# Performance work log

Hardware: AMD Instinct MI355X
Metric: run time of the kernel (lower is better)

## Reference

```python
import jax, jax.numpy as jnp
import numpy as np

B, C, D, H, W = 2, 512, 32, 32, 32
L, CTX = 256, 768
NH, HD, G = 8, 64, 8
EPS = 1e-5


def group_norm(x, w, b):
    Bb, Cc, Dd, Hh, Ww = x.shape
    xg = x.reshape(Bb, G, Cc // G, Dd, Hh, Ww)
    mu = xg.mean(axis=(2, 3, 4, 5), keepdims=True)
    var = xg.var(axis=(2, 3, 4, 5), keepdims=True)
    xn = ((xg - mu) * jax.lax.rsqrt(var + EPS)).reshape(Bb, Cc, Dd, Hh, Ww)
    return xn * w[None, :, None, None, None] + b[None, :, None, None, None]


def layer_norm(x, w, b):
    mu = x.mean(axis=-1, keepdims=True)
    var = x.var(axis=-1, keepdims=True)
    return (x - mu) * jax.lax.rsqrt(var + EPS) * w + b


def setup_inputs() -> dict:
    key = jax.random.key(0)
    ks = jax.random.split(key, 8)
    s = 0.02  # weight init scale
    return {
        "x": jax.random.normal(ks[0], (B, C, D, H, W), jnp.float32),
        "context": jax.random.normal(ks[1], (B, L, CTX), jnp.float32),
        "gn_w": jnp.ones((C,), jnp.float32),
        "gn_b": jnp.zeros((C,), jnp.float32),
        "ln_w": jnp.ones((CTX,), jnp.float32),
        "ln_b": jnp.zeros((CTX,), jnp.float32),
        "q_w": jax.random.normal(ks[2], (C, C), jnp.float32) * s,
        "q_b": jnp.zeros((C,), jnp.float32),
        "k_w": jax.random.normal(ks[3], (C, CTX), jnp.float32) * s,
        "k_b": jnp.zeros((C,), jnp.float32),
        "v_w": jax.random.normal(ks[4], (C, CTX), jnp.float32) * s,
        "v_b": jnp.zeros((C,), jnp.float32),
        "proj_w": jax.random.normal(ks[5], (C, C), jnp.float32) * s,
        "proj_b": jnp.zeros((C,), jnp.float32),
    }


def reference(x, context, gn_w, gn_b, ln_w, ln_b, q_w, q_b, k_w, k_b, v_w, v_b, proj_w, proj_b):
    Bb, Cc, Dd, Hh, Ww = x.shape
    S = Dd * Hh * Ww
    h = group_norm(x, gn_w, gn_b)
    ctx = layer_norm(context, ln_w, ln_b)
    # 1x1 Conv3d == per-voxel linear over channels
    q = jnp.einsum('oc,bcdhw->bodhw', q_w, h) + q_b[None, :, None, None, None]
    q = q.reshape(Bb, NH, HD, S)                                        # (b,h,e,s)
    k = (ctx @ k_w.T + k_b).reshape(Bb, L, NH, HD).transpose(0, 2, 1, 3)  # (b,h,l,e)
    v = (ctx @ v_w.T + v_b).reshape(Bb, L, NH, HD).transpose(0, 2, 1, 3)  # (b,h,l,e)
    scale = HD ** -0.5
    attn = jnp.einsum('bhes,bhle->bhsl', q, k) * scale                  # (b,h,S,L)
    attn = jax.nn.softmax(attn, axis=-1)
    out = jnp.einsum('bhsl,bhle->bhes', attn, v).reshape(Bb, Cc, Dd, Hh, Ww)
    out = jnp.einsum('oc,bcdhw->bodhw', proj_w, out) + proj_b[None, :, None, None, None]
    return out + x
```

## Files before the change

kernel.cpp:

```cpp
#include <hip/hip_runtime.h>

typedef unsigned short u16;
typedef unsigned int u32;
typedef __attribute__((ext_vector_type(4))) float f32x4;
typedef __attribute__((ext_vector_type(8))) short bf16x8;
typedef __attribute__((ext_vector_type(8))) u16 u16x8;
typedef __attribute__((ext_vector_type(4))) u16 u16x4;
typedef __attribute__((ext_vector_type(4))) u32 u32x4;

#define DEVI __device__ __forceinline__

constexpr int C_ = 512, S_ = 32768, L_ = 256, CTX_ = 768;

DEVI u16 f2b(float f) {
    union { float f; unsigned u; } x; x.f = f;
    unsigned r = x.u + 0x7fffu + ((x.u >> 16) & 1u);
    return (u16)(r >> 16);
}

DEVI f32x4 mfma16(bf16x8 a, bf16x8 b, f32x4 c) {
    return __builtin_amdgcn_mfma_f32_16x16x32_bf16(a, b, c, 0, 0, 0);
}

DEVI void gload16(const void* g, void* l) {
    __builtin_amdgcn_global_load_lds(
        (const __attribute__((address_space(1))) void*)g,
        (__attribute__((address_space(3))) void*)l, 16, 0, 0);
}

DEVI u32 cvtpk(float lo, float hi) {
    u32 d;
    asm("v_cvt_pk_bf16_f32 %0, %1, %2" : "=v"(d) : "v"(lo), "v"(hi));
    return d;
}
DEVI void pl32(u32& a, u32& b) {
    asm volatile("v_permlane32_swap_b32 %0, %1" : "+v"(a), "+v"(b));
}
DEVI void pl16(u32& a, u32& b) {
    asm volatile("v_permlane16_swap_b32 %0, %1" : "+v"(a), "+v"(b));
}

__global__ __launch_bounds__(256) void cvt_w(
    const float* __restrict__ a0, const float* __restrict__ a1,
    const float* __restrict__ a2, const float* __restrict__ a3,
    u16* __restrict__ o0, u16* __restrict__ o1,
    u16* __restrict__ o2, u16* __restrict__ o3)
{
    int which = blockIdx.y;
    const float* src = which == 0 ? a0 : which == 1 ? a1 : which == 2 ? a2 : a3;
    u16* dst = which == 0 ? o0 : which == 1 ? o1 : which == 2 ? o2 : o3;
    int n4 = (which == 1 || which == 2) ? (512 * 768 / 4) : (512 * 512 / 4);
    int i = blockIdx.x * 256 + threadIdx.x;
    if (i < n4) {
        float4 v = ((const float4*)src)[i];
        u16x4 o; o[0] = f2b(v.x); o[1] = f2b(v.y); o[2] = f2b(v.z); o[3] = f2b(v.w);
        ((u16x4*)dst)[i] = o;
    }
}

__global__ __launch_bounds__(256) void gn_partial(const float* __restrict__ x,
                                                  float* __restrict__ part)
{
    const int bg = blockIdx.y, blk = blockIdx.x, tid = threadIdx.x;
    const float* base = x + (size_t)bg * 64 * S_ + (size_t)blk * 1024 + tid * 4;
    float s1 = 0.f, s2 = 0.f;
    for (int c = 0; c < 64; ++c) {
        float4 v = *(const float4*)(base + (size_t)c * S_);
        s1 += v.x + v.y + v.z + v.w;
        s2 += v.x * v.x + v.y * v.y + v.z * v.z + v.w * v.w;
    }
    for (int m = 1; m < 64; m <<= 1) { s1 += __shfl_xor(s1, m); s2 += __shfl_xor(s2, m); }
    __shared__ float a1[4], a2[4];
    int w = tid >> 6, lane = tid & 63;
    if (lane == 0) { a1[w] = s1; a2[w] = s2; }
    __syncthreads();
    if (tid == 0) {
        part[(bg * 32 + blk) * 2 + 0] = a1[0] + a1[1] + a1[2] + a1[3];
        part[(bg * 32 + blk) * 2 + 1] = a2[0] + a2[1] + a2[2] + a2[3];
    }
}

__global__ __launch_bounds__(64) void gn_final(const float* __restrict__ part,
                                               float* __restrict__ stats)
{
    int bg = blockIdx.x, tid = threadIdx.x;
    float s1 = tid < 32 ? part[(bg * 32 + tid) * 2] : 0.f;
    float s2 = tid < 32 ? part[(bg * 32 + tid) * 2 + 1] : 0.f;
    for (int m = 1; m < 32; m <<= 1) { s1 += __shfl_xor(s1, m); s2 += __shfl_xor(s2, m); }
    if (tid == 0) {
        const float invN = 1.0f / (64.0f * (float)S_);
        float mu = s1 * invN, var = s2 * invN - mu * mu;
        stats[bg * 2] = mu;
        stats[bg * 2 + 1] = rsqrtf(var + 1e-5f);
    }
}

__global__ __launch_bounds__(256) void gn_coef(
    const float* __restrict__ stats, const float* __restrict__ gw,
    const float* __restrict__ gb, float* __restrict__ ca, float* __restrict__ cb)
{
    int i = blockIdx.x * 256 + threadIdx.x;
    int z = i >> 9, c = i & 511;
    int bg = z * 8 + (c >> 6);
    float mu = stats[bg * 2], rs = stats[bg * 2 + 1];
    float a = rs * gw[c];
    ca[i] = a;
    cb[i] = gb[c] - mu * a;
}

__global__ __launch_bounds__(256) void ln_ctx(
    const float* __restrict__ ctx, const float* __restrict__ lw,
    const float* __restrict__ lb, u16* __restrict__ cn)
{
    const int row = blockIdx.x, tid = threadIdx.x;
    const float* p = ctx + (size_t)row * CTX_;
    float v0 = p[tid], v1 = p[tid + 256], v2 = p[tid + 512];
    float s1 = v0 + v1 + v2, s2 = v0 * v0 + v1 * v1 + v2 * v2;
    for (int m = 1; m < 64; m <<= 1) { s1 += __shfl_xor(s1, m); s2 += __shfl_xor(s2, m); }
    __shared__ float a1[4], a2[4];
    int w = tid >> 6, lane = tid & 63;
    if (lane == 0) { a1[w] = s1; a2[w] = s2; }
    __syncthreads();
    s1 = a1[0] + a1[1] + a1[2] + a1[3];
    s2 = a2[0] + a2[1] + a2[2] + a2[3];
    const float invN = 1.0f / 768.0f;
    float mu = s1 * invN, rstd = rsqrtf(s2 * invN - mu * mu + 1e-5f);
    u16* o = cn + (size_t)row * CTX_;
    o[tid]       = f2b((v0 - mu) * rstd * lw[tid]       + lb[tid]);
    o[tid + 256] = f2b((v1 - mu) * rstd * lw[tid + 256] + lb[tid + 256]);
    o[tid + 512] = f2b((v2 - mu) * rstd * lw[tid + 512] + lb[tid + 512]);
}

template <int MODE, bool SWAP>
__global__ __launch_bounds__(256, 4) void gemm_nt(
    const u16* __restrict__ A, const u16* __restrict__ Bp,
    const float* __restrict__ bias, void* __restrict__ outp,
    const float* __restrict__ resid, int K, int ldo,
    size_t aStride, size_t bStride, size_t oStride, float scale,
    const u16* __restrict__ Bp2, const float* __restrict__ bias2,
    void* __restrict__ outp2)
{
    __shared__ __align__(16) u16 lA[2][4096];
    __shared__ __align__(16) u16 lB[2][4096];
    const int tid = threadIdx.x;
    const int w = tid >> 6, lane = tid & 63;
    const int g = lane >> 4, r = lane & 15;

    const int nx = gridDim.x, nxy = nx * gridDim.y;
    const int raw = blockIdx.x + nx * blockIdx.y;
    const int tile = (raw & 7) * (nxy >> 3) + (raw >> 3);
    const int bx = tile % nx, by = tile / nx;
    const int m0 = (SWAP ? by : bx) * 128, n0 = (SWAP ? bx : by) * 128;
    const int z = blockIdx.z;
    A += (size_t)z * aStride;
    const u16* Bsel = Bp;
    if constexpr (MODE == 3) { if (z) Bsel = Bp2; }
    Bsel += (size_t)z * bStride;

    const int l8 = lane & 7, lh = lane >> 3;
    const int u_ = l8 ^ lh;
    const int mro = (lh << 1) + (u_ >> 2);
    const int kco = (u_ & 3) * 8;
    const int wr = w >> 1, wc = w & 1;
    const int nt = K >> 5;

    f32x4 acc[4][4];
#pragma unroll
    for (int m = 0; m < 4; ++m)
#pragma unroll
        for (int n = 0; n < 4; ++n) acc[m][n] = f32x4{0.f, 0.f, 0.f, 0.f};

#define STAGE_B(t, bi_) {                                                      \
    size_t ko_ = (size_t)((t) * 32 + kco);                                     \
    _Pragma("unroll")                                                          \
    for (int j = 0; j < 2; ++j) {                                              \
        int grow_ = w * 32 + j * 16 + mro;                                     \
        gload16(Bsel + (size_t)(n0 + grow_) * K + ko_,                         \
                &lB[bi_][(w * 16 + j * 8) << 6]);                              \
    } }

#define STAGE_A(t, bi_) {                                                      \
    size_t ko_ = (size_t)((t) * 32 + kco);                                     \
    _Pragma("unroll")                                                          \
    for (int j = 0; j < 2; ++j) {                                              \
        int grow_ = w * 32 + j * 16 + mro;                                     \
        gload16(A + (size_t)(m0 + grow_) * K + ko_,                            \
                &lA[bi_][(w * 16 + j * 8) << 6]);                              \
    } }

    const float* xA = nullptr;
    const float* cAp = nullptr;
    const float* cBp = nullptr;
    int cp2 = 0, sb = 0, zc = 0;
    f32x4 a00{}, a01{}, a10{}, a11{};
    float2 ka{}, kb{};
    if constexpr (MODE == 4) {
        xA = resid + (size_t)z * ((size_t)C_ * S_);
        cAp = bias2;
        cBp = (const float*)outp2;
        cp2 = (tid >> 4) * 2;
        sb = (tid & 15) * 8;
        zc = z * 512;
    }

#define LOAD_A4(t) {                                                           \
    int c0n_ = (t) * 32 + cp2;                                                 \
    const float* r0_ = xA + (size_t)c0n_ * S_ + m0 + sb;                       \
    a00 = *(const f32x4*)r0_;  a01 = *(const f32x4*)(r0_ + 4);                 \
    a10 = *(const f32x4*)(r0_ + S_); a11 = *(const f32x4*)(r0_ + S_ + 4);      \
    ka = *(const float2*)&cAp[zc + c0n_];                                      \
    kb = *(const float2*)&cBp[zc + c0n_]; }

#define WRITE_A4(bi_) {                                                        \
    _Pragma("unroll")                                                          \
    for (int j = 0; j < 8; ++j) {                                              \
        float v0_ = ((j < 4) ? a00[j] : a01[j - 4]) * ka.x + kb.x;             \
        float v1_ = ((j < 4) ? a10[j] : a11[j - 4]) * ka.y + kb.y;             \
        int mm_ = sb + j;                                                      \
        int idx_ = ((mm_ >> 1) << 6)                                           \
            + (((((mm_ & 1) << 2) + (cp2 >> 3)) ^ ((mm_ >> 1) & 7)) << 3)      \
            + (cp2 & 7);                                                       \
        *(u32*)&lA[bi_][idx_] = cvtpk(v0_, v1_);                               \
    } }

    if constexpr (MODE == 4) {
        STAGE_B(0, 0);
        LOAD_A4(0);
        WRITE_A4(0);
    } else {
        STAGE_A(0, 0);
        STAGE_B(0, 0);
    }
    __syncthreads();

    for (int t = 0; t < nt; ++t) {
        const int cur = t & 1;
        if (t + 1 < nt) {
            STAGE_B(t + 1, cur ^ 1);
            if constexpr (MODE == 4) { LOAD_A4(t + 1); }
            else                     { STAGE_A(t + 1, cur ^ 1); }
        }
        bf16x8 af[4], bf_[4];
#pragma unroll
        for (int m = 0; m < 4; ++m) {
            int row = wr * 32 + m * 8 + (r >> 1);
            int slot = (((r & 1) << 2) + g) ^ ((r >> 1) & 7);
            af[m] = *(const bf16x8*)&lA[cur][(row << 6) + (slot << 3)];
        }
#pragma unroll
        for (int n = 0; n < 4; ++n) {
            int row = wc * 32 + n * 8 + (r >> 1);
            int slot = (((r & 1) << 2) + g) ^ ((r >> 1) & 7);
            bf_[n] = *(const bf16x8*)&lB[cur][(row << 6) + (slot << 3)];
        }
#pragma unroll
        for (int m = 0; m < 4; ++m)
#pragma unroll
            for (int n = 0; n < 4; ++n)
                acc[m][n] = mfma16(bf_[n], af[m], acc[m][n]);
        if constexpr (MODE == 4) { if (t + 1 < nt) WRITE_A4(cur ^ 1); }
        __syncthreads();
    }
#undef STAGE_A
#undef STAGE_B
#undef LOAD_A4
#undef WRITE_A4

    if constexpr (MODE == 0 || MODE == 4) {
        u16* ob = (u16*)outp + (size_t)z * oStride;
#pragma unroll
        for (int m = 0; m < 4; ++m) {
            int gm = m0 + wr * 64 + m * 16 + r;
#pragma unroll
            for (int n = 0; n < 4; ++n) {
                int gn0 = n0 + wc * 64 + n * 16 + g * 4;
                float4 bn = *(const float4*)&bias[gn0];
                u32 w0 = cvtpk(acc[m][n][0] * scale + bn.x * scale,
                               acc[m][n][1] * scale + bn.y * scale);
                u32 w1 = cvtpk(acc[m][n][2] * scale + bn.z * scale,
                               acc[m][n][3] * scale + bn.w * scale);
                *(uint2*)&ob[(size_t)gm * ldo + gn0] = make_uint2(w0, w1);
            }
        }
    } else if constexpr (MODE == 2) {
        float* of = (float*)outp + (size_t)z * oStride;
        const float* rs = resid + (size_t)z * oStride;
#pragma unroll
        for (int m = 0; m < 4; ++m) {
            int gm = m0 + wr * 64 + m * 16 + r;
            float bm = bias[gm];
#pragma unroll
            for (int n = 0; n < 4; ++n) {
                int gn0 = n0 + wc * 64 + n * 16 + g * 4;
                size_t idx = (size_t)gm * ldo + gn0;
                float4 rv = *(const float4*)&rs[idx];
                float4 o4;
                o4.x = acc[m][n][0] + bm + rv.x;
                o4.y = acc[m][n][1] + bm + rv.y;
                o4.z = acc[m][n][2] + bm + rv.z;
                o4.w = acc[m][n][3] + bm + rv.w;
                *(float4*)&of[idx] = o4;
            }
        }
    } else if constexpr (MODE == 3) {
        if (z == 0) {
            u16* ob = (u16*)outp;
#pragma unroll
            for (int m = 0; m < 4; ++m) {
                int gm = m0 + wr * 64 + m * 16 + r;
#pragma unroll
                for (int n = 0; n < 4; ++n) {
                    int gn0 = n0 + wc * 64 + n * 16 + g * 4;
                    float4 bn = *(const float4*)&bias[gn0];
                    u32 w0 = cvtpk(acc[m][n][0] + bn.x, acc[m][n][1] + bn.y);
                    u32 w1 = cvtpk(acc[m][n][2] + bn.z, acc[m][n][3] + bn.w);
                    *(uint2*)&ob[(size_t)gm * ldo + gn0] = make_uint2(w0, w1);
                }
            }
        } else {
            u16* ob = (u16*)outp2;
#pragma unroll
            for (int m = 0; m < 4; ++m) {
                int gm = m0 + wr * 64 + m * 16 + r;
                int bb = gm >> 8, l = gm & 255;
#pragma unroll
                for (int n = 0; n < 4; ++n) {
                    int gn0 = n0 + wc * 64 + n * 16 + g * 4;
#pragma unroll
                    for (int i = 0; i < 4; ++i)
                        ob[((size_t)(bb * 512 + gn0 + i)) * 256 + l] =
                            f2b(acc[m][n][i] + bias2[gn0 + i]);
                }
            }
        }
    }
}

__global__ __launch_bounds__(256, 2) void attn_kernel(
    const u16* __restrict__ q, const u16* __restrict__ kk,
    const u16* __restrict__ vv, u16* __restrict__ ao)
{
    __shared__ __align__(16) u16 sm[32768];
    const int tid = threadIdx.x;
    const int w = tid >> 6, lane = tid & 63;
    const int g = lane >> 4, r = lane & 15;
    const int bh = blockIdx.y, b = bh >> 3, h = bh & 7;
    const int s0 = blockIdx.x * 128;

    {
        const u16* kbase = kk + ((size_t)b * L_) * C_ + h * 64;
#pragma unroll
        for (int j = 0; j < 8; ++j) {
            int idx = j * 256 + tid;
            int l = idx >> 3, ch = idx & 7;
            u16x8 val = *(const u16x8*)(kbase + (size_t)l * C_ + ch * 8);
            *(u16x8*)&sm[l * 64 + ((ch ^ (l & 7)) << 3)] = val;
        }
        const u16* vbase = vv + ((size_t)bh * 64) * 256;
#pragma unroll
        for (int j = 0; j < 8; ++j) {
            int idx = j * 256 + tid;
            int e = idx >> 5, ch = idx & 31;
            u16x8 val = *(const u16x8*)(vbase + (size_t)e * 256 + ch * 8);
            *(u16x8*)&sm[16384 + e * 256 + ((ch ^ (e & 7)) << 3)] = val;
        }
    }

    const int sw = s0 + w * 32;
    bf16x8 qf[2][2];
#pragma unroll
    for (int m = 0; m < 2; ++m)
#pragma unroll
        for (int kt = 0; kt < 2; ++kt)
            qf[m][kt] = *(const bf16x8*)(q + ((size_t)(b * S_ + sw + m * 16 + r)) * C_
                                         + h * 64 + kt * 32 + g * 8);
    __syncthreads();

    f32x4 accs[2][16];
#pragma unroll
    for (int m = 0; m < 2; ++m)
#pragma unroll
        for (int n = 0; n < 16; ++n) accs[m][n] = f32x4{0.f, 0.f, 0.f, 0.f};
    __builtin_amdgcn_s_setprio(1);
#pragma unroll
    for (int n = 0; n < 16; ++n) {
#pragma unroll
        for (int kt = 0; kt < 2; ++kt) {
            int c = kt * 4 + g;
            bf16x8 kf = *(const bf16x8*)&sm[(n * 16 + r) * 64 + ((c ^ (r & 7)) << 3)];
#pragma unroll
            for (int m = 0; m < 2; ++m) accs[m][n] = mfma16(kf, qf[m][kt], accs[m][n]);
        }
    }
    __builtin_amdgcn_s_setprio(0);

    float inv[2];
#pragma unroll
    for (int m = 0; m < 2; ++m) {
        float mx = accs[m][0][0];
#pragma unroll
        for (int n = 0; n < 16; ++n)
#pragma unroll
            for (int i = 0; i < 4; ++i) mx = fmaxf(mx, accs[m][n][i]);
        mx = fmaxf(mx, __shfl_xor(mx, 16));
        mx = fmaxf(mx, __shfl_xor(mx, 32));
        float sum = 0.f;
#pragma unroll
        for (int n = 0; n < 16; ++n)
#pragma unroll
            for (int i = 0; i < 4; ++i) {
                float e = __expf(accs[m][n][i] - mx);
                accs[m][n][i] = e; sum += e;
            }
        sum += __shfl_xor(sum, 16);
        sum += __shfl_xor(sum, 32);
        inv[m] = 1.0f / sum;
    }

    f32x4 acco[2][4];
#pragma unroll
    for (int m = 0; m < 2; ++m)
#pragma unroll
        for (int n = 0; n < 4; ++n) acco[m][n] = f32x4{0.f, 0.f, 0.f, 0.f};

#pragma unroll
    for (int c = 0; c < 8; ++c) {
        bf16x8 pa[2];
#pragma unroll
        for (int m = 0; m < 2; ++m) {
            u32 x0 = cvtpk(accs[m][2 * c][0] * inv[m], accs[m][2 * c][1] * inv[m]);
            u32 x1 = cvtpk(accs[m][2 * c][2] * inv[m], accs[m][2 * c][3] * inv[m]);
            u32 y0 = cvtpk(accs[m][2 * c + 1][0] * inv[m], accs[m][2 * c + 1][1] * inv[m]);
            u32 y1 = cvtpk(accs[m][2 * c + 1][2] * inv[m], accs[m][2 * c + 1][3] * inv[m]);
            pl32(x0, y0);
            pl32(x1, y1);
            pl16(x0, y0);
            pl16(x1, y1);
            u32x4 pw; pw[0] = x0; pw[1] = x1; pw[2] = y0; pw[3] = y1;
            pa[m] = *(bf16x8*)&pw;
        }
        bf16x8 vf[4];
#pragma unroll
        for (int n = 0; n < 4; ++n) {
            int e = n * 16 + r;
            vf[n] = *(const bf16x8*)&sm[16384 + e * 256 + (((c * 4 + g) ^ (r & 7)) << 3)];
        }
        __builtin_amdgcn_s_setprio(1);
#pragma unroll
        for (int m = 0; m < 2; ++m)
#pragma unroll
            for (int n = 0; n < 4; ++n)
                acco[m][n] = mfma16(vf[n], pa[m], acco[m][n]);
        __builtin_amdgcn_s_setprio(0);
    }

#pragma unroll
    for (int m = 0; m < 2; ++m) {
        const size_t rowb = ((size_t)(b * S_ + sw + m * 16 + r)) * C_ + h * 64;
#pragma unroll
        for (int n = 0; n < 4; ++n) {
            u32 w0 = cvtpk(acco[m][n][0], acco[m][n][1]);
            u32 w1 = cvtpk(acco[m][n][2], acco[m][n][3]);
            *(uint2*)&ao[rowb + n * 16 + g * 4] = make_uint2(w0, w1);
        }
    }
}

extern "C" void kernel_launch(void* const* d_in, const int* in_sizes, int n_in,
                              void* d_out, int out_size, void* d_ws, size_t ws_size,
                              hipStream_t stream)
{
    (void)in_sizes; (void)n_in; (void)out_size; (void)ws_size;
    const float* x    = (const float*)d_in[0];
    const float* ctx  = (const float*)d_in[1];
    const float* gn_w = (const float*)d_in[2];
    const float* gn_b = (const float*)d_in[3];
    const float* ln_w = (const float*)d_in[4];
    const float* ln_b = (const float*)d_in[5];
    const float* q_w  = (const float*)d_in[6];
    const float* q_b  = (const float*)d_in[7];
    const float* k_w  = (const float*)d_in[8];
    const float* k_b  = (const float*)d_in[9];
    const float* v_w  = (const float*)d_in[10];
    const float* v_b  = (const float*)d_in[11];
    const float* p_w  = (const float*)d_in[12];
    const float* p_b  = (const float*)d_in[13];
    float* out = (float*)d_out;

    char* ws = (char*)d_ws;
    constexpr size_t WS_WQ   = 0;
    constexpr size_t WS_WK   = WS_WQ + (size_t)512 * 512 * 2;
    constexpr size_t WS_WV   = WS_WK + (size_t)512 * 768 * 2;
    constexpr size_t WS_WP   = WS_WV + (size_t)512 * 768 * 2;
    constexpr size_t WS_PART = WS_WP + (size_t)512 * 512 * 2;
    constexpr size_t WS_STAT = WS_PART + (size_t)16 * 64 * 2 * 4;
    constexpr size_t WS_CA   = WS_STAT + 256;
    constexpr size_t WS_CB   = WS_CA + 4096;
    constexpr size_t WS_CTXN = WS_CB + 4096;
    constexpr size_t WS_K    = WS_CTXN + (size_t)512 * 768 * 2;
    constexpr size_t WS_V    = WS_K + (size_t)2 * 8 * 256 * 64 * 2;
    constexpr size_t WS_Q    = WS_V + (size_t)2 * 8 * 256 * 64 * 2;
    constexpr size_t WS_H    = WS_Q + (size_t)2 * 32768 * 512 * 2;

    u16* wq = (u16*)(ws + WS_WQ);
    u16* wk = (u16*)(ws + WS_WK);
    u16* wv = (u16*)(ws + WS_WV);
    u16* wp = (u16*)(ws + WS_WP);
    float* part  = (float*)(ws + WS_PART);
    float* stats = (float*)(ws + WS_STAT);
    float* coefA = (float*)(ws + WS_CA);
    float* coefB = (float*)(ws + WS_CB);
    u16* ctxn = (u16*)(ws + WS_CTXN);
    u16* kt   = (u16*)(ws + WS_K);
    u16* vt   = (u16*)(ws + WS_V);
    u16* qt   = (u16*)(ws + WS_Q);
    u16* ao   = (u16*)(ws + WS_H);

    const size_t bsc = (size_t)S_ * C_;

    cvt_w<<<dim3(384, 4), 256, 0, stream>>>(q_w, k_w, v_w, p_w, wq, wk, wv, wp);
    gn_partial<<<dim3(32, 16), 256, 0, stream>>>(x, part);
    gn_final<<<16, 64, 0, stream>>>(part, stats);
    gn_coef<<<4, 256, 0, stream>>>(stats, gn_w, gn_b, coefA, coefB);
    ln_ctx<<<512, 256, 0, stream>>>(ctx, ln_w, ln_b, ctxn);
    gemm_nt<4, true><<<dim3(4, 256, 2), 256, 0, stream>>>(
        nullptr, wq, q_b, qt, x, 512, 512, 0, 0, bsc, 0.125f,
        nullptr, coefA, coefB);
    gemm_nt<3, false><<<dim3(4, 4, 2), 256, 0, stream>>>(
        ctxn, wk, k_b, kt, nullptr, 768, 512, 0, 0, 0, 1.0f,
        wv, v_b, vt);
    attn_kernel<<<dim3(256, 16), 256, 0, stream>>>(qt, kt, vt, ao);
    gemm_nt<2, false><<<dim3(4, 256, 2), 256, 0, stream>>>(
        wp, ao, p_b, out, x, 512, S_, 0, bsc, bsc, 1.0f,
        nullptr, nullptr, nullptr);
}
```

Measured before the change: 273.6 us.

## Merge small prep kernels, enlarge attention blocks, raise GEMM occupancy hint

Fuses weight conversion and context layer norm into one launch, and fuses group-norm finalization with coefficient computation, removing two kernel launches and an intermediate stats buffer. The attention kernel now runs 512 threads per block covering 256 queries, so K/V tiles staged in shared memory are shared by twice as many waves. The GEMM launch bound is raised to 5 blocks per CU, which may force register spills.

```diff
diff --git a/kernel.cpp b/kernel.cpp
--- a/kernel.cpp
+++ b/kernel.cpp
@@ -40,22 +40,44 @@
     asm volatile("v_permlane16_swap_b32 %0, %1" : "+v"(a), "+v"(b));
 }
 
-__global__ __launch_bounds__(256) void cvt_w(
+__global__ __launch_bounds__(256) void prep_small(
     const float* __restrict__ a0, const float* __restrict__ a1,
     const float* __restrict__ a2, const float* __restrict__ a3,
     u16* __restrict__ o0, u16* __restrict__ o1,
-    u16* __restrict__ o2, u16* __restrict__ o3)
+    u16* __restrict__ o2, u16* __restrict__ o3,
+    const float* __restrict__ ctx, const float* __restrict__ lw,
+    const float* __restrict__ lb, u16* __restrict__ cn)
 {
-    int which = blockIdx.y;
-    const float* src = which == 0 ? a0 : which == 1 ? a1 : which == 2 ? a2 : a3;
-    u16* dst = which == 0 ? o0 : which == 1 ? o1 : which == 2 ? o2 : o3;
-    int n4 = (which == 1 || which == 2) ? (512 * 768 / 4) : (512 * 512 / 4);
-    int i = blockIdx.x * 256 + threadIdx.x;
-    if (i < n4) {
-        float4 v = ((const float4*)src)[i];
-        u16x4 o; o[0] = f2b(v.x); o[1] = f2b(v.y); o[2] = f2b(v.z); o[3] = f2b(v.w);
-        ((u16x4*)dst)[i] = o;
-    }
+    const int which = blockIdx.y, tid = threadIdx.x;
+    if (which < 4) {
+        const float* src = which == 0 ? a0 : which == 1 ? a1 : which == 2 ? a2 : a3;
+        u16* dst = which == 0 ? o0 : which == 1 ? o1 : which == 2 ? o2 : o3;
+        int n4 = (which == 1 || which == 2) ? (512 * 768 / 4) : (512 * 512 / 4);
+        int i = blockIdx.x * 256 + tid;
+        if (i < n4) {
+            float4 v = ((const float4*)src)[i];
+            u16x4 o; o[0] = f2b(v.x); o[1] = f2b(v.y); o[2] = f2b(v.z); o[3] = f2b(v.w);
+            ((u16x4*)dst)[i] = o;
+        }
+        return;
+    }
+    const int row = blockIdx.x;
+    const float* p = ctx + (size_t)row * CTX_;
+    float v0 = p[tid], v1 = p[tid + 256], v2 = p[tid + 512];
+    float s1 = v0 + v1 + v2, s2 = v0 * v0 + v1 * v1 + v2 * v2;
+    for (int m = 1; m < 64; m <<= 1) { s1 += __shfl_xor(s1, m); s2 += __shfl_xor(s2, m); }
+    __shared__ float a1s[4], a2s[4];
+    int w = tid >> 6, lane = tid & 63;
+    if (lane == 0) { a1s[w] = s1; a2s[w] = s2; }
+    __syncthreads();
+    s1 = a1s[0] + a1s[1] + a1s[2] + a1s[3];
+    s2 = a2s[0] + a2s[1] + a2s[2] + a2s[3];
+    const float invN = 1.0f / 768.0f;
+    float mu = s1 * invN, rstd = rsqrtf(s2 * invN - mu * mu + 1e-5f);
+    u16* o = cn + (size_t)row * CTX_;
+    o[tid]       = f2b((v0 - mu) * rstd * lw[tid]       + lb[tid]);
+    o[tid + 256] = f2b((v1 - mu) * rstd * lw[tid + 256] + lb[tid + 256]);
+    o[tid + 512] = f2b((v2 - mu) * rstd * lw[tid + 512] + lb[tid + 512]);
 }
 
 __global__ __launch_bounds__(256) void gn_partial(const float* __restrict__ x,
@@ -80,59 +102,26 @@
     }
 }
 
-__global__ __launch_bounds__(64) void gn_final(const float* __restrict__ part,
-                                               float* __restrict__ stats)
+__global__ __launch_bounds__(64) void gn_final_coef(
+    const float* __restrict__ part, const float* __restrict__ gw,
+    const float* __restrict__ gb, float* __restrict__ ca, float* __restrict__ cb)
 {
     int bg = blockIdx.x, tid = threadIdx.x;
     float s1 = tid < 32 ? part[(bg * 32 + tid) * 2] : 0.f;
     float s2 = tid < 32 ? part[(bg * 32 + tid) * 2 + 1] : 0.f;
     for (int m = 1; m < 32; m <<= 1) { s1 += __shfl_xor(s1, m); s2 += __shfl_xor(s2, m); }
-    if (tid == 0) {
-        const float invN = 1.0f / (64.0f * (float)S_);
-        float mu = s1 * invN, var = s2 * invN - mu * mu;
-        stats[bg * 2] = mu;
-        stats[bg * 2 + 1] = rsqrtf(var + 1e-5f);
-    }
-}
-
-__global__ __launch_bounds__(256) void gn_coef(
-    const float* __restrict__ stats, const float* __restrict__ gw,
-    const float* __restrict__ gb, float* __restrict__ ca, float* __restrict__ cb)
-{
-    int i = blockIdx.x * 256 + threadIdx.x;
-    int z = i >> 9, c = i & 511;
-    int bg = z * 8 + (c >> 6);
-    float mu = stats[bg * 2], rs = stats[bg * 2 + 1];
+    const float invN = 1.0f / (64.0f * (float)S_);
+    float mu = __shfl(s1, 0) * invN;
+    float var = __shfl(s2, 0) * invN - mu * mu;
+    float rs = rsqrtf(var + 1e-5f);
+    int z = bg >> 3, c = (bg & 7) * 64 + tid;
     float a = rs * gw[c];
-    ca[i] = a;
-    cb[i] = gb[c] - mu * a;
-}
-
-__global__ __launch_bounds__(256) void ln_ctx(
-    const float* __restrict__ ctx, const float* __restrict__ lw,
-    const float* __restrict__ lb, u16* __restrict__ cn)
-{
-    const int row = blockIdx.x, tid = threadIdx.x;
-    const float* p = ctx + (size_t)row * CTX_;
-    float v0 = p[tid], v1 = p[tid + 256], v2 = p[tid + 512];
-    float s1 = v0 + v1 + v2, s2 = v0 * v0 + v1 * v1 + v2 * v2;
-    for (int m = 1; m < 64; m <<= 1) { s1 += __shfl_xor(s1, m); s2 += __shfl_xor(s2, m); }
-    __shared__ float a1[4], a2[4];
-    int w = tid >> 6, lane = tid & 63;
-    if (lane == 0) { a1[w] = s1; a2[w] = s2; }
-    __syncthreads();
-    s1 = a1[0] + a1[1] + a1[2] + a1[3];
-    s2 = a2[0] + a2[1] + a2[2] + a2[3];
-    const float invN = 1.0f / 768.0f;
-    float mu = s1 * invN, rstd = rsqrtf(s2 * invN - mu * mu + 1e-5f);
-    u16* o = cn + (size_t)row * CTX_;
-    o[tid]       = f2b((v0 - mu) * rstd * lw[tid]       + lb[tid]);
-    o[tid + 256] = f2b((v1 - mu) * rstd * lw[tid + 256] + lb[tid + 256]);
-    o[tid + 512] = f2b((v2 - mu) * rstd * lw[tid + 512] + lb[tid + 512]);
+    ca[z * 512 + c] = a;
+    cb[z * 512 + c] = gb[c] - mu * a;
 }
 
 template <int MODE, bool SWAP>
-__global__ __launch_bounds__(256, 4) void gemm_nt(
+__global__ __launch_bounds__(256, 5) void gemm_nt(
     const u16* __restrict__ A, const u16* __restrict__ Bp,
     const float* __restrict__ bias, void* __restrict__ outp,
     const float* __restrict__ resid, int K, int ldo,
@@ -336,7 +325,7 @@
     }
 }
 
-__global__ __launch_bounds__(256, 2) void attn_kernel(
+__global__ __launch_bounds__(512, 4) void attn_kernel(
     const u16* __restrict__ q, const u16* __restrict__ kk,
     const u16* __restrict__ vv, u16* __restrict__ ao)
 {
@@ -345,21 +334,21 @@
     const int w = tid >> 6, lane = tid & 63;
     const int g = lane >> 4, r = lane & 15;
     const int bh = blockIdx.y, b = bh >> 3, h = bh & 7;
-    const int s0 = blockIdx.x * 128;
+    const int s0 = blockIdx.x * 256;
 
     {
         const u16* kbase = kk + ((size_t)b * L_) * C_ + h * 64;
 #pragma unroll
-        for (int j = 0; j < 8; ++j) {
-            int idx = j * 256 + tid;
+        for (int j = 0; j < 4; ++j) {
+            int idx = j * 512 + tid;
             int l = idx >> 3, ch = idx & 7;
             u16x8 val = *(const u16x8*)(kbase + (size_t)l * C_ + ch * 8);
             *(u16x8*)&sm[l * 64 + ((ch ^ (l & 7)) << 3)] = val;
         }
         const u16* vbase = vv + ((size_t)bh * 64) * 256;
 #pragma unroll
-        for (int j = 0; j < 8; ++j) {
-            int idx = j * 256 + tid;
+        for (int j = 0; j < 4; ++j) {
+            int idx = j * 512 + tid;
             int e = idx >> 5, ch = idx & 31;
             u16x8 val = *(const u16x8*)(vbase + (size_t)e * 256 + ch * 8);
             *(u16x8*)&sm[16384 + e * 256 + ((ch ^ (e & 7)) << 3)] = val;
@@ -493,8 +482,7 @@
     constexpr size_t WS_WV   = WS_WK + (size_t)512 * 768 * 2;
     constexpr size_t WS_WP   = WS_WV + (size_t)512 * 768 * 2;
     constexpr size_t WS_PART = WS_WP + (size_t)512 * 512 * 2;
-    constexpr size_t WS_STAT = WS_PART + (size_t)16 * 64 * 2 * 4;
-    constexpr size_t WS_CA   = WS_STAT + 256;
+    constexpr size_t WS_CA   = WS_PART + (size_t)16 * 64 * 2 * 4;
     constexpr size_t WS_CB   = WS_CA + 4096;
     constexpr size_t WS_CTXN = WS_CB + 4096;
     constexpr size_t WS_K    = WS_CTXN + (size_t)512 * 768 * 2;
@@ -507,7 +495,6 @@
     u16* wv = (u16*)(ws + WS_WV);
     u16* wp = (u16*)(ws + WS_WP);
     float* part  = (float*)(ws + WS_PART);
-    float* stats = (float*)(ws + WS_STAT);
     float* coefA = (float*)(ws + WS_CA);
     float* coefB = (float*)(ws + WS_CB);
     u16* ctxn = (u16*)(ws + WS_CTXN);
@@ -518,18 +505,18 @@
 
     const size_t bsc = (size_t)S_ * C_;
 
-    cvt_w<<<dim3(384, 4), 256, 0, stream>>>(q_w, k_w, v_w, p_w, wq, wk, wv, wp);
     gn_partial<<<dim3(32, 16), 256, 0, stream>>>(x, part);
-    gn_final<<<16, 64, 0, stream>>>(part, stats);
-    gn_coef<<<4, 256, 0, stream>>>(stats, gn_w, gn_b, coefA, coefB);
-    ln_ctx<<<512, 256, 0, stream>>>(ctx, ln_w, ln_b, ctxn);
+    prep_small<<<dim3(512, 5), 256, 0, stream>>>(q_w, k_w, v_w, p_w,
+                                                 wq, wk, wv, wp,
+                                                 ctx, ln_w, ln_b, ctxn);
+    gn_final_coef<<<16, 64, 0, stream>>>(part, gn_w, gn_b, coefA, coefB);
     gemm_nt<4, true><<<dim3(4, 256, 2), 256, 0, stream>>>(
         nullptr, wq, q_b, qt, x, 512, 512, 0, 0, bsc, 0.125f,
         nullptr, coefA, coefB);
     gemm_nt<3, false><<<dim3(4, 4, 2), 256, 0, stream>>>(
         ctxn, wk, k_b, kt, nullptr, 768, 512, 0, 0, 0, 1.0f,
         wv, v_b, vt);
-    attn_kernel<<<dim3(256, 16), 256, 0, stream>>>(qt, kt, vt, ao);
+    attn_kernel<<<dim3(128, 16), 512, 0, stream>>>(qt, kt, vt, ao);
     gemm_nt<2, false><<<dim3(4, 256, 2), 256, 0, stream>>>(
         wp, ao, p_b, out, x, 512, S_, 0, bsc, bsc, 1.0f,
         nullptr, nullptr, nullptr);
```

Measured after the change: 692.3 us. 2.53x slower.
